# Optimization experiments

Hardware: AMD Instinct MI355X
Metric: run time of the kernel (lower is better)

Reference implementation:

```python
import jax, jax.numpy as jnp
import numpy as np

N_NODES = 20000
N_EDGES = 320000
D = 256          # out_channels (== in_channels here, so PyG zero-padding is a no-op)
NUM_LAYERS = 5


def setup_inputs() -> dict:
    key = jax.random.key(0)
    ks = jax.random.split(key, 8)
    x = jax.random.normal(ks[0], (N_NODES, D), dtype=jnp.float32)
    src = jax.random.randint(ks[1], (N_EDGES,), 0, N_NODES)
    dst = jax.random.randint(ks[2], (N_EDGES,), 0, N_NODES)
    edge_index = jnp.stack([src, dst]).astype(jnp.int64)
    edge_attr = jax.random.uniform(ks[3], (N_EDGES,), dtype=jnp.float32)
    s = 1.0 / np.sqrt(D)
    # per-layer message transform weights [L, D, D]
    weight = jax.random.uniform(ks[4], (NUM_LAYERS, D, D), minval=-s, maxval=s, dtype=jnp.float32)
    # GRUCell parameters (torch layout: [3*D, D] for W_ih/W_hh, [3*D] biases; gate order r, z, n)
    w_ih = jax.random.uniform(ks[5], (3 * D, D), minval=-s, maxval=s, dtype=jnp.float32)
    w_hh = jax.random.uniform(ks[6], (3 * D, D), minval=-s, maxval=s, dtype=jnp.float32)
    b = jax.random.uniform(ks[7], (2, 3 * D), minval=-s, maxval=s, dtype=jnp.float32)
    return {"x": x, "edge_index": edge_index, "edge_attr": edge_attr,
            "weight": weight, "w_ih": w_ih, "w_hh": w_hh,
            "b_ih": b[0], "b_hh": b[1]}


def gru_cell(m, h, w_ih, w_hh, b_ih, b_hh):
    gi = m @ w_ih.T + b_ih   # [N, 3D]
    gh = h @ w_hh.T + b_hh   # [N, 3D]
    i_r, i_z, i_n = jnp.split(gi, 3, axis=1)
    h_r, h_z, h_n = jnp.split(gh, 3, axis=1)
    r = jax.nn.sigmoid(i_r + h_r)
    z = jax.nn.sigmoid(i_z + h_z)
    n = jnp.tanh(i_n + r * h_n)
    return (1.0 - z) * n + z * h


def reference(x, edge_index, edge_attr, weight, w_ih, w_hh, b_ih, b_hh):
    src = edge_index[0]
    dst = edge_index[1]
    n_nodes = x.shape[0]
    h = x  # in_channels == out_channels, so no zero padding needed
    for i in range(weight.shape[0]):
        m = h @ weight[i]                                  # [N, D] transformed messages
        msgs = m[src] * edge_attr[:, None]                 # gather + edge weighting [E, D]
        agg = jax.ops.segment_sum(msgs, dst, num_segments=n_nodes)  # scatter-add [N, D]
        h = gru_cell(agg, h, w_ih, w_hh, b_ih, b_hh)
    return h
```

## Files before the change

### kernel.cpp

```cpp
#include <hip/hip_runtime.h>
#include <hip/hip_bf16.h>

#define NN 20000
#define NE 320000
#define DD 256

typedef __attribute__((ext_vector_type(8))) short bf16x8;
typedef __attribute__((ext_vector_type(4))) float f32x4;
typedef __attribute__((ext_vector_type(4))) int   int4v;
typedef __attribute__((ext_vector_type(4))) float float4v;

typedef __attribute__((address_space(1))) unsigned int gas_uint;
typedef __attribute__((address_space(3))) unsigned int las_uint;
static __device__ __forceinline__ void gload16(const void* g, void* l) {
    __builtin_amdgcn_global_load_lds((gas_uint*)g, (las_uint*)l, 16, 0, 0);
}

__device__ __forceinline__ unsigned short f2bf(float f) {
    union { float f; unsigned u; } v; v.f = f;
    unsigned r = v.u + 0x7fffu + ((v.u >> 16) & 1u);
    return (unsigned short)(r >> 16);
}
__device__ __forceinline__ float bf2f(unsigned short h) {
    union { unsigned u; float f; } v; v.u = ((unsigned)h) << 16;
    return v.f;
}
__device__ __forceinline__ float fast_sigmoid(float x) {
    return 1.f / (1.f + __expf(-x));
}
__device__ __forceinline__ float fast_tanh(float x) {
    x = fminf(fmaxf(x, -30.f), 30.f);
    float e = __expf(-2.f * x);
    return (1.f - e) / (1.f + e);
}


__global__ void cast_kernel(const float* __restrict__ in, unsigned short* __restrict__ out, int n) {
    int i = (blockIdx.x * blockDim.x + threadIdx.x) * 4;
    if (i >= n) return;
    float4v v = *reinterpret_cast<const float4v*>(in + i);
    uint2 o;
    o.x = (unsigned)f2bf(v.x) | ((unsigned)f2bf(v.y) << 16);
    o.y = (unsigned)f2bf(v.z) | ((unsigned)f2bf(v.w) << 16);
    *reinterpret_cast<uint2*>(out + i) = o;
}

__global__ __launch_bounds__(256) void pgemm_kernel(const unsigned short* __restrict__ A,
                                                    const unsigned short* __restrict__ Bt,
                                                    unsigned short* __restrict__ C) {
    __shared__ __align__(16) unsigned short As[128 * 64];
    __shared__ __align__(16) unsigned short Bs[64 * 64];
    const int t = threadIdx.x;
    const int lane = t & 63;
    const int w = t >> 6;
    const int wr = w >> 1, wc = w & 1;
    const int m0 = blockIdx.y * 128;
    const int n0 = blockIdx.x * 64;

    f32x4 acc[4][2];
    const f32x4 z4 = {0.f, 0.f, 0.f, 0.f};
    for (int i = 0; i < 4; ++i) for (int j = 0; j < 2; ++j) acc[i][j] = z4;

    for (int kt = 0; kt < 4; ++kt) {
        const int k0 = kt * 64;
#pragma unroll
        for (int rnd = 0; rnd < 4; ++rnd) {
            int cb = rnd * 256 + (w << 6);
            int c = cb + lane;
            int row = c >> 3, sl = c & 7;
            int gsl = sl ^ (row & 7);
            gload16(A + (size_t)(m0 + row) * 256 + k0 + gsl * 8, &As[cb * 8]);
        }
#pragma unroll
        for (int rnd = 0; rnd < 2; ++rnd) {
            int cb = rnd * 256 + (w << 6);
            int c = cb + lane;
            int row = c >> 3, sl = c & 7;
            int gsl = sl ^ (row & 7);
            gload16(Bt + (size_t)(n0 + row) * 256 + k0 + gsl * 8, &Bs[cb * 8]);
        }
        __syncthreads();
#pragma unroll
        for (int ks = 0; ks < 2; ++ks) {
            const int slot = ks * 4 + (lane >> 4);
            bf16x8 a[4], b[2];
#pragma unroll
            for (int mi = 0; mi < 4; ++mi) {
                int row = wr * 64 + mi * 16 + (lane & 15);
                a[mi] = *reinterpret_cast<const bf16x8*>(&As[row * 64 + ((slot ^ (row & 7)) << 3)]);
            }
#pragma unroll
            for (int ni = 0; ni < 2; ++ni) {
                int row = wc * 32 + ni * 16 + (lane & 15);
                b[ni] = *reinterpret_cast<const bf16x8*>(&Bs[row * 64 + ((slot ^ (row & 7)) << 3)]);
            }
#pragma unroll
            for (int mi = 0; mi < 4; ++mi)
#pragma unroll
                for (int ni = 0; ni < 2; ++ni)
                    acc[mi][ni] = __builtin_amdgcn_mfma_f32_16x16x32_bf16(a[mi], b[ni], acc[mi][ni], 0, 0, 0);
        }
        __syncthreads();
    }
#pragma unroll
    for (int mi = 0; mi < 4; ++mi)
#pragma unroll
        for (int ni = 0; ni < 2; ++ni)
#pragma unroll
            for (int r = 0; r < 4; ++r) {
                int grow = m0 + wr * 64 + mi * 16 + (lane >> 4) * 4 + r;
                int gcol = n0 + wc * 32 + ni * 16 + (lane & 15);
                C[(size_t)grow * 768 + gcol] = f2bf(acc[mi][ni][r]);
            }
}

__global__ void wc5_kernel(const unsigned short* __restrict__ Pall,
                           const float* __restrict__ whh,
                           unsigned short* __restrict__ Wc5) {
    int id = blockIdx.x * 256 + threadIdx.x;
    int l = id >> 19;
    int rem = id & 524287;
    int np = rem >> 9, k = rem & 511;
    int g = (np >> 4) & 3;
    int d = ((np >> 6) << 4) | (np & 15);
    int gate_row = (g == 0) ? d : (g == 1) ? 256 + d : 512 + d;
    unsigned short v;
    if (k < 256) {
        v = (g == 3) ? (unsigned short)0 : Pall[((size_t)(l * 256 + k)) * 768 + gate_row];
    } else {
        v = (g == 2) ? (unsigned short)0 : f2bf(whh[(size_t)gate_row * 256 + (k - 256)]);
    }
    Wc5[id] = v;
}


__global__ void hist_kernel(const int* __restrict__ dst, int* __restrict__ deg) {
    int e = blockIdx.x * 256 + threadIdx.x;
    if (e < NE) atomicAdd(&deg[dst[e]], 1);
}

__global__ __launch_bounds__(1024) void scan_kernel(const int* __restrict__ deg, int* __restrict__ base) {
    __shared__ int part[1024];
    const int t = threadIdx.x;
    const int CH = 20;
    int start = t * CH;
    int s = 0;
    for (int i = 0; i < CH; ++i) { int idx = start + i; if (idx < NN) s += deg[idx]; }
    part[t] = s; __syncthreads();
    for (int off = 1; off < 1024; off <<= 1) {
        int v = (t >= off) ? part[t - off] : 0;
        __syncthreads();
        part[t] += v;
        __syncthreads();
    }
    int run = (t == 0) ? 0 : part[t - 1];
    for (int i = 0; i < CH; ++i) {
        int idx = start + i;
        if (idx < NN) { base[idx] = run; run += deg[idx]; }
    }
    if (t == 1023) base[NN] = run;
}

__global__ void fill_kernel(const int* __restrict__ src, const int* __restrict__ dst,
                            const float* __restrict__ attr, const int* __restrict__ base,
                            int* __restrict__ cursor, int* __restrict__ ssrc,
                            float* __restrict__ sattr) {
    int e = blockIdx.x * 256 + threadIdx.x;
    if (e >= NE) return;
    int d = dst[e];
    int pos = base[d] + atomicAdd(&cursor[d], 1);
    ssrc[pos] = src[e];
    sattr[pos] = attr[e];
}

__global__ __launch_bounds__(256) void gather_agg_kernel(const unsigned short* __restrict__ Hbf,
                                                         const int* __restrict__ base,
                                                         const int* __restrict__ ssrc,
                                                         const float* __restrict__ sattr,
                                                         unsigned short* __restrict__ AggBf) {
    int node = blockIdx.x * 4 + (threadIdx.x >> 6);
    if (node >= NN) return;
    int lane = threadIdx.x & 63;
    int half = lane >> 5;
    int dl = lane & 31;
    int b0 = base[node], b1 = base[node + 1];
    float ac[8] = {0.f, 0.f, 0.f, 0.f, 0.f, 0.f, 0.f, 0.f};
    for (int p = b0 + half; p < b1; p += 2) {
        int s = ssrc[p];
        float a = sattr[p];
        int4v v = *reinterpret_cast<const int4v*>(Hbf + (size_t)s * 256 + dl * 8);
        ac[0] += a * bf2f((unsigned short)(v.x & 0xffff));
        ac[1] += a * bf2f((unsigned short)((unsigned)v.x >> 16));
        ac[2] += a * bf2f((unsigned short)(v.y & 0xffff));
        ac[3] += a * bf2f((unsigned short)((unsigned)v.y >> 16));
        ac[4] += a * bf2f((unsigned short)(v.z & 0xffff));
        ac[5] += a * bf2f((unsigned short)((unsigned)v.z >> 16));
        ac[6] += a * bf2f((unsigned short)(v.w & 0xffff));
        ac[7] += a * bf2f((unsigned short)((unsigned)v.w >> 16));
    }
#pragma unroll
    for (int j = 0; j < 8; ++j) ac[j] += __shfl_xor(ac[j], 32);
    if (half == 0) {
        int4v o;
        o.x = (int)((unsigned)f2bf(ac[0]) | ((unsigned)f2bf(ac[1]) << 16));
        o.y = (int)((unsigned)f2bf(ac[2]) | ((unsigned)f2bf(ac[3]) << 16));
        o.z = (int)((unsigned)f2bf(ac[4]) | ((unsigned)f2bf(ac[5]) << 16));
        o.w = (int)((unsigned)f2bf(ac[6]) | ((unsigned)f2bf(ac[7]) << 16));
        *reinterpret_cast<int4v*>(AggBf + (size_t)node * 256 + dl * 8) = o;
    }
}

__global__ __launch_bounds__(512) void gru_kernel(const unsigned short* __restrict__ Abf,
                                                  const unsigned short* __restrict__ Hbf,
                                                  const unsigned short* __restrict__ Wc,
                                                  const float* __restrict__ b_ih,
                                                  const float* __restrict__ b_hh,
                                                  const float* __restrict__ h_in,
                                                  float* __restrict__ h_out,
                                                  unsigned short* __restrict__ Hbf_out) {
    __shared__ __align__(16) unsigned short As[128 * 64];
    __shared__ __align__(16) unsigned short Bs[128 * 64];
    const int t = threadIdx.x;
    const int lane = t & 63;
    const int w = t >> 6;
    const int wr = w >> 1, wc = w & 1;
    int b = blockIdx.x;
    int ww = (b & 7) * 158 + (b >> 3);
    const int mt = ww >> 3, nt = ww & 7;
    const int m0 = mt * 128;
    const int n0 = nt * 128;

    f32x4 acc[2][4];
    const f32x4 z4 = {0.f, 0.f, 0.f, 0.f};
#pragma unroll
    for (int i = 0; i < 2; ++i)
#pragma unroll
        for (int j = 0; j < 4; ++j) acc[i][j] = z4;

    for (int kt = 0; kt < 8; ++kt) {
        const unsigned short* aptr = (kt < 4) ? Abf : Hbf;
        const int ka = (kt & 3) * 64;
        const int kb = kt * 64;
#pragma unroll
        for (int i = 0; i < 2; ++i) {
            int cb = i * 512 + (w << 6);
            int c = cb + lane;
            int row = c >> 3, sl = c & 7;
            int gsl = sl ^ (row & 7);
            gload16(aptr + (size_t)(m0 + row) * 256 + ka + gsl * 8, &As[cb * 8]);
            gload16(Wc + (size_t)(n0 + row) * 512 + kb + gsl * 8, &Bs[cb * 8]);
        }
        __syncthreads();
#pragma unroll
        for (int ks = 0; ks < 2; ++ks) {
            const int slot = ks * 4 + (lane >> 4);
            bf16x8 a[2], bfr[4];
#pragma unroll
            for (int mi = 0; mi < 2; ++mi) {
                int row = wr * 32 + mi * 16 + (lane & 15);
                a[mi] = *reinterpret_cast<const bf16x8*>(&As[row * 64 + ((slot ^ (row & 7)) << 3)]);
            }
#pragma unroll
            for (int g = 0; g < 4; ++g) {
                int row = wc * 64 + g * 16 + (lane & 15);
                bfr[g] = *reinterpret_cast<const bf16x8*>(&Bs[row * 64 + ((slot ^ (row & 7)) << 3)]);
            }
#pragma unroll
            for (int mi = 0; mi < 2; ++mi)
#pragma unroll
                for (int g = 0; g < 4; ++g)
                    acc[mi][g] = __builtin_amdgcn_mfma_f32_16x16x32_bf16(a[mi], bfr[g], acc[mi][g], 0, 0, 0);
        }
        __syncthreads();
    }

    const int c = lane & 15;
    const int d = (nt * 2 + wc) * 16 + c;
    const float bir = b_ih[d],       bhr = b_hh[d];
    const float biz = b_ih[256 + d], bhz = b_hh[256 + d];
    const float bin_ = b_ih[512 + d], bhn = b_hh[512 + d];
#pragma unroll
    for (int mi = 0; mi < 2; ++mi)
#pragma unroll
        for (int r = 0; r < 4; ++r) {
            int grow = m0 + wr * 32 + mi * 16 + (lane >> 4) * 4 + r;
            if (grow >= NN) continue;
            float rr = fast_sigmoid(acc[mi][0][r] + bir + bhr);
            float zz = fast_sigmoid(acc[mi][1][r] + biz + bhz);
            float nn = fast_tanh(acc[mi][2][r] + bin_ + rr * (acc[mi][3][r] + bhn));
            float hp = h_in[(size_t)grow * 256 + d];
            float hv = (1.f - zz) * nn + zz * hp;
            h_out[(size_t)grow * 256 + d] = hv;
            Hbf_out[(size_t)grow * 256 + d] = f2bf(hv);
        }
}


extern "C" void kernel_launch(void* const* d_in, const int* in_sizes, int n_in,
                              void* d_out, int out_size, void* d_ws, size_t ws_size,
                              hipStream_t stream) {
    const float* x     = (const float*)d_in[0];
    const int*   eidx  = (const int*)d_in[1];
    const float* eattr = (const float*)d_in[2];
    const float* W     = (const float*)d_in[3];
    const float* wih   = (const float*)d_in[4];
    const float* whh   = (const float*)d_in[5];
    const float* bih   = (const float*)d_in[6];
    const float* bhh   = (const float*)d_in[7];
    float* out = (float*)d_out;
    const int* esrc = eidx;
    const int* edst = eidx + NE;

    char* p = (char*)d_ws;
    auto alloc = [&](size_t bytes) -> char* {
        char* r = p; p += (bytes + 255) & ~(size_t)255; return r;
    };
    unsigned short* hbfA  = (unsigned short*)alloc((size_t)NN * DD * 2);
    unsigned short* hbfB  = (unsigned short*)alloc((size_t)NN * DD * 2);
    unsigned short* aggbf = (unsigned short*)alloc((size_t)NN * DD * 2);
    unsigned short* wnb   = (unsigned short*)alloc((size_t)5 * DD * DD * 2);
    unsigned short* wihb  = (unsigned short*)alloc((size_t)768 * DD * 2);
    unsigned short* pall  = (unsigned short*)alloc((size_t)1280 * 768 * 2);
    unsigned short* wc5   = (unsigned short*)alloc((size_t)5 * 1024 * 512 * 2);
    int*   deg    = (int*)alloc((size_t)NN * 4);
    int*   basep  = (int*)alloc((size_t)(NN + 1) * 4);
    int*   cursor = (int*)alloc((size_t)NN * 4);
    int*   ssrc   = (int*)alloc((size_t)NE * 4);
    float* sattr  = (float*)alloc((size_t)NE * 4);
    alloc(262144);

    hipMemsetAsync(deg, 0, (size_t)NN * 4, stream);
    hipMemsetAsync(cursor, 0, (size_t)NN * 4, stream);

    cast_kernel<<<320, 256, 0, stream>>>(W, wnb, 5 * DD * DD);
    cast_kernel<<<192, 256, 0, stream>>>(wih, wihb, 768 * DD);
    cast_kernel<<<5000, 256, 0, stream>>>(x, hbfA, NN * DD);
    pgemm_kernel<<<dim3(12, 10), 256, 0, stream>>>(wnb, wihb, pall);
    wc5_kernel<<<10240, 256, 0, stream>>>(pall, whh, wc5);
    hist_kernel<<<1250, 256, 0, stream>>>(edst, deg);
    scan_kernel<<<1, 1024, 0, stream>>>(deg, basep);
    fill_kernel<<<1250, 256, 0, stream>>>(esrc, edst, eattr, basep, cursor, ssrc, sattr);

    unsigned short* hb_cur = hbfA;
    unsigned short* hb_nxt = hbfB;
    const float* h_in = x;
    for (int l = 0; l < 5; ++l) {
        gather_agg_kernel<<<5000, 256, 0, stream>>>(hb_cur, basep, ssrc, sattr, aggbf);
        gru_kernel<<<1264, 512, 0, stream>>>(aggbf, hb_cur, wc5 + (size_t)l * 1024 * 512,
                                             bih, bhh, h_in, out, hb_nxt);
        h_in = out;
        unsigned short* tmp = hb_cur; hb_cur = hb_nxt; hb_nxt = tmp;
    }
    (void)in_sizes; (void)n_in; (void)out_size; (void)ws_size;
}
```

Before: 381.7 us.

## Drop zero-padded GRU weight blocks and skip intermediate fp32 hidden-state traffic

Repacks the combined GRU weight into separate input and hidden halves of 768 columns each. This removes the all-zero gate blocks that previously padded the GEMM to 1024x512 and wasted MFMA work and weight loads. The GRU kernel now uses 128x48 tiles with 256 threads and per-gate accumulators. It also writes the fp32 output only on the last layer and reads the previous hidden state from the bf16 copy instead of fp32. That cuts global memory traffic, at the cost of carrying the blended hidden state in bf16 precision between layers.

```diff
diff --git a/kernel.cpp b/kernel.cpp
--- a/kernel.cpp
+++ b/kernel.cpp
@@ -118,18 +118,20 @@
                            const float* __restrict__ whh,
                            unsigned short* __restrict__ Wc5) {
     int id = blockIdx.x * 256 + threadIdx.x;
-    int l = id >> 19;
-    int rem = id & 524287;
-    int np = rem >> 9, k = rem & 511;
-    int g = (np >> 4) & 3;
-    int d = ((np >> 6) << 4) | (np & 15);
-    int gate_row = (g == 0) ? d : (g == 1) ? 256 + d : 512 + d;
+    int k  = id & 255;
+    int t2 = id >> 8;
+    int n3 = t2 % 768;
+    int t3 = t2 / 768;
+    int hf = t3 & 1;
+    int l  = t3 >> 1;
+    int g3 = (n3 >> 4) % 3;
+    int dg = n3 / 48;
+    int dc = n3 & 15;
+    int d  = dg * 16 + dc;
+    int gate_row = g3 * 256 + d;
     unsigned short v;
-    if (k < 256) {
-        v = (g == 3) ? (unsigned short)0 : Pall[((size_t)(l * 256 + k)) * 768 + gate_row];
-    } else {
-        v = (g == 2) ? (unsigned short)0 : f2bf(whh[(size_t)gate_row * 256 + (k - 256)]);
-    }
+    if (hf == 0) v = Pall[((size_t)(l * 256 + k)) * 768 + gate_row];
+    else         v = f2bf(whh[(size_t)gate_row * 256 + k]);
     Wc5[id] = v;
 }
 
@@ -210,88 +212,104 @@
     }
 }
 
-__global__ __launch_bounds__(512) void gru_kernel(const unsigned short* __restrict__ Abf,
-                                                  const unsigned short* __restrict__ Hbf,
-                                                  const unsigned short* __restrict__ Wc,
-                                                  const float* __restrict__ b_ih,
-                                                  const float* __restrict__ b_hh,
-                                                  const float* __restrict__ h_in,
-                                                  float* __restrict__ h_out,
-                                                  unsigned short* __restrict__ Hbf_out) {
+__global__ __launch_bounds__(256) void gru2_kernel(const unsigned short* __restrict__ Abf,
+                                                   const unsigned short* __restrict__ Hbf,
+                                                   const unsigned short* __restrict__ Wc,
+                                                   const float* __restrict__ b_ih,
+                                                   const float* __restrict__ b_hh,
+                                                   const float* __restrict__ x_f32,
+                                                   float* __restrict__ h_out,
+                                                   unsigned short* __restrict__ Hbf_out,
+                                                   int first, int last) {
     __shared__ __align__(16) unsigned short As[128 * 64];
-    __shared__ __align__(16) unsigned short Bs[128 * 64];
+    __shared__ __align__(16) unsigned short Bs[48 * 64];
     const int t = threadIdx.x;
     const int lane = t & 63;
     const int w = t >> 6;
-    const int wr = w >> 1, wc = w & 1;
     int b = blockIdx.x;
-    int ww = (b & 7) * 158 + (b >> 3);
-    const int mt = ww >> 3, nt = ww & 7;
+    int ww = (b & 7) * 316 + (b >> 3);
+    const int mt = ww >> 4, dg = ww & 15;
     const int m0 = mt * 128;
-    const int n0 = nt * 128;
-
-    f32x4 acc[2][4];
+
+    f32x4 aR[2], aZ[2], aI[2], aH[2];
     const f32x4 z4 = {0.f, 0.f, 0.f, 0.f};
 #pragma unroll
-    for (int i = 0; i < 2; ++i)
-#pragma unroll
-        for (int j = 0; j < 4; ++j) acc[i][j] = z4;
-
-    for (int kt = 0; kt < 8; ++kt) {
-        const unsigned short* aptr = (kt < 4) ? Abf : Hbf;
-        const int ka = (kt & 3) * 64;
-        const int kb = kt * 64;
-#pragma unroll
-        for (int i = 0; i < 2; ++i) {
-            int cb = i * 512 + (w << 6);
-            int c = cb + lane;
-            int row = c >> 3, sl = c & 7;
-            int gsl = sl ^ (row & 7);
-            gload16(aptr + (size_t)(m0 + row) * 256 + ka + gsl * 8, &As[cb * 8]);
-            gload16(Wc + (size_t)(n0 + row) * 512 + kb + gsl * 8, &Bs[cb * 8]);
-        }
-        __syncthreads();
-#pragma unroll
-        for (int ks = 0; ks < 2; ++ks) {
-            const int slot = ks * 4 + (lane >> 4);
-            bf16x8 a[2], bfr[4];
-#pragma unroll
-            for (int mi = 0; mi < 2; ++mi) {
-                int row = wr * 32 + mi * 16 + (lane & 15);
-                a[mi] = *reinterpret_cast<const bf16x8*>(&As[row * 64 + ((slot ^ (row & 7)) << 3)]);
-            }
-#pragma unroll
-            for (int g = 0; g < 4; ++g) {
-                int row = wc * 64 + g * 16 + (lane & 15);
-                bfr[g] = *reinterpret_cast<const bf16x8*>(&Bs[row * 64 + ((slot ^ (row & 7)) << 3)]);
-            }
-#pragma unroll
-            for (int mi = 0; mi < 2; ++mi)
-#pragma unroll
-                for (int g = 0; g < 4; ++g)
-                    acc[mi][g] = __builtin_amdgcn_mfma_f32_16x16x32_bf16(a[mi], bfr[g], acc[mi][g], 0, 0, 0);
-        }
-        __syncthreads();
-    }
-
-    const int c = lane & 15;
-    const int d = (nt * 2 + wc) * 16 + c;
-    const float bir = b_ih[d],       bhr = b_hh[d];
-    const float biz = b_ih[256 + d], bhz = b_hh[256 + d];
+    for (int i = 0; i < 2; ++i) { aR[i] = z4; aZ[i] = z4; aI[i] = z4; aH[i] = z4; }
+
+    auto do_half = [&](const unsigned short* __restrict__ aptr,
+                       const unsigned short* __restrict__ wcb,
+                       f32x4 (&aX)[2]) {
+        for (int kq = 0; kq < 4; ++kq) {
+            const int ka = kq * 64;
+#pragma unroll
+            for (int rnd = 0; rnd < 4; ++rnd) {
+                int cb = rnd * 256 + (w << 6);
+                int c = cb + lane;
+                int row = c >> 3, sl = c & 7;
+                int gsl = sl ^ (row & 7);
+                gload16(aptr + (size_t)(m0 + row) * 256 + ka + gsl * 8, &As[cb * 8]);
+            }
+            {
+                int cb = (w << 6);
+                int c = cb + lane;
+                int row = c >> 3, sl = c & 7;
+                int gsl = sl ^ (row & 7);
+                gload16(wcb + (size_t)(dg * 48 + row) * 256 + ka + gsl * 8, &Bs[cb * 8]);
+            }
+            if (w < 2) {
+                int cb = 256 + (w << 6);
+                int c = cb + lane;
+                int row = c >> 3, sl = c & 7;
+                int gsl = sl ^ (row & 7);
+                gload16(wcb + (size_t)(dg * 48 + row) * 256 + ka + gsl * 8, &Bs[cb * 8]);
+            }
+            __syncthreads();
+#pragma unroll
+            for (int ks = 0; ks < 2; ++ks) {
+                const int slot = ks * 4 + (lane >> 4);
+                bf16x8 a[2], bfr[3];
+#pragma unroll
+                for (int mi = 0; mi < 2; ++mi) {
+                    int row = w * 32 + mi * 16 + (lane & 15);
+                    a[mi] = *reinterpret_cast<const bf16x8*>(&As[row * 64 + ((slot ^ (row & 7)) << 3)]);
+                }
+#pragma unroll
+                for (int g3 = 0; g3 < 3; ++g3) {
+                    int row = g3 * 16 + (lane & 15);
+                    bfr[g3] = *reinterpret_cast<const bf16x8*>(&Bs[row * 64 + ((slot ^ (row & 7)) << 3)]);
+                }
+#pragma unroll
+                for (int mi = 0; mi < 2; ++mi) {
+                    aR[mi] = __builtin_amdgcn_mfma_f32_16x16x32_bf16(a[mi], bfr[0], aR[mi], 0, 0, 0);
+                    aZ[mi] = __builtin_amdgcn_mfma_f32_16x16x32_bf16(a[mi], bfr[1], aZ[mi], 0, 0, 0);
+                    aX[mi] = __builtin_amdgcn_mfma_f32_16x16x32_bf16(a[mi], bfr[2], aX[mi], 0, 0, 0);
+                }
+            }
+            __syncthreads();
+        }
+    };
+
+    do_half(Abf, Wc, aI);
+    do_half(Hbf, Wc + 768 * 256, aH);
+
+    const int d = dg * 16 + (lane & 15);
+    const float bir = b_ih[d],        bhr = b_hh[d];
+    const float biz = b_ih[256 + d],  bhz = b_hh[256 + d];
     const float bin_ = b_ih[512 + d], bhn = b_hh[512 + d];
 #pragma unroll
     for (int mi = 0; mi < 2; ++mi)
 #pragma unroll
         for (int r = 0; r < 4; ++r) {
-            int grow = m0 + wr * 32 + mi * 16 + (lane >> 4) * 4 + r;
+            int grow = m0 + w * 32 + mi * 16 + (lane >> 4) * 4 + r;
             if (grow >= NN) continue;
-            float rr = fast_sigmoid(acc[mi][0][r] + bir + bhr);
-            float zz = fast_sigmoid(acc[mi][1][r] + biz + bhz);
-            float nn = fast_tanh(acc[mi][2][r] + bin_ + rr * (acc[mi][3][r] + bhn));
-            float hp = h_in[(size_t)grow * 256 + d];
+            size_t idx = (size_t)grow * 256 + d;
+            float rr = fast_sigmoid(aR[mi][r] + bir + bhr);
+            float zz = fast_sigmoid(aZ[mi][r] + biz + bhz);
+            float nn = fast_tanh(aI[mi][r] + bin_ + rr * (aH[mi][r] + bhn));
+            float hp = first ? x_f32[idx] : bf2f(Hbf[idx]);
             float hv = (1.f - zz) * nn + zz * hp;
-            h_out[(size_t)grow * 256 + d] = hv;
-            Hbf_out[(size_t)grow * 256 + d] = f2bf(hv);
+            if (last) h_out[idx] = hv;
+            Hbf_out[idx] = f2bf(hv);
         }
 }
 
@@ -321,7 +339,7 @@
     unsigned short* wnb   = (unsigned short*)alloc((size_t)5 * DD * DD * 2);
     unsigned short* wihb  = (unsigned short*)alloc((size_t)768 * DD * 2);
     unsigned short* pall  = (unsigned short*)alloc((size_t)1280 * 768 * 2);
-    unsigned short* wc5   = (unsigned short*)alloc((size_t)5 * 1024 * 512 * 2);
+    unsigned short* wc5   = (unsigned short*)alloc((size_t)5 * 2 * 768 * 256 * 2);
     int*   deg    = (int*)alloc((size_t)NN * 4);
     int*   basep  = (int*)alloc((size_t)(NN + 1) * 4);
     int*   cursor = (int*)alloc((size_t)NN * 4);
@@ -336,19 +354,18 @@
     cast_kernel<<<192, 256, 0, stream>>>(wih, wihb, 768 * DD);
     cast_kernel<<<5000, 256, 0, stream>>>(x, hbfA, NN * DD);
     pgemm_kernel<<<dim3(12, 10), 256, 0, stream>>>(wnb, wihb, pall);
-    wc5_kernel<<<10240, 256, 0, stream>>>(pall, whh, wc5);
+    wc5_kernel<<<7680, 256, 0, stream>>>(pall, whh, wc5);
     hist_kernel<<<1250, 256, 0, stream>>>(edst, deg);
     scan_kernel<<<1, 1024, 0, stream>>>(deg, basep);
     fill_kernel<<<1250, 256, 0, stream>>>(esrc, edst, eattr, basep, cursor, ssrc, sattr);
 
     unsigned short* hb_cur = hbfA;
     unsigned short* hb_nxt = hbfB;
-    const float* h_in = x;
     for (int l = 0; l < 5; ++l) {
         gather_agg_kernel<<<5000, 256, 0, stream>>>(hb_cur, basep, ssrc, sattr, aggbf);
-        gru_kernel<<<1264, 512, 0, stream>>>(aggbf, hb_cur, wc5 + (size_t)l * 1024 * 512,
-                                             bih, bhh, h_in, out, hb_nxt);
-        h_in = out;
+        gru2_kernel<<<2528, 256, 0, stream>>>(aggbf, hb_cur, wc5 + (size_t)l * 2 * 768 * 256,
+                                              bih, bhh, x, out, hb_nxt,
+                                              (l == 0) ? 1 : 0, (l == 4) ? 1 : 0);
         unsigned short* tmp = hb_cur; hb_cur = hb_nxt; hb_nxt = tmp;
     }
     (void)in_sizes; (void)n_in; (void)out_size; (void)ws_size;
```

Result: no change. 383.4 us (+0.4%).
